# Performance work log

Hardware: AMD Instinct MI355X
Metric: run time of the kernel (lower is better)

Reference implementation:

```python
import jax, jax.numpy as jnp
import numpy as np

B, I_LEN, Q_LEN, H = 256, 256, 64, 512
MID, G, FLAT_OUT = 512, 1, 1024


def setup_inputs() -> dict:
    key = jax.random.key(0)
    ks = jax.random.split(key, 20)
    s = lambda k, sh: jax.random.normal(k, sh, dtype=jnp.float32) * 0.02
    inp = {
        'i_batch': jax.random.normal(ks[0], (B, I_LEN, H), dtype=jnp.float32),
        'q_batch': jax.random.normal(ks[1], (B, Q_LEN, H), dtype=jnp.float32),
        'i_mask': jax.random.bernoulli(ks[2], 0.1, (B, 1, 1, I_LEN)),
        'q_mask': jax.random.bernoulli(ks[3], 0.1, (B, 1, 1, Q_LEN)),
        # l_flatten (applied to i_feat) params
        'lf_w1': s(ks[4], (H, MID)), 'lf_b1': jnp.zeros((MID,), jnp.float32),
        'lf_w2': s(ks[5], (MID, G)), 'lf_b2': jnp.zeros((G,), jnp.float32),
        'lf_wm': s(ks[6], (H * G, FLAT_OUT)), 'lf_bm': jnp.zeros((FLAT_OUT,), jnp.float32),
        # i_flatten (applied to l_feat) params
        'if_w1': s(ks[7], (H, MID)), 'if_b1': jnp.zeros((MID,), jnp.float32),
        'if_w2': s(ks[8], (MID, G)), 'if_b2': jnp.zeros((G,), jnp.float32),
        'if_wm': s(ks[9], (H * G, FLAT_OUT)), 'if_bm': jnp.zeros((FLAT_OUT,), jnp.float32),
        # fh_h: Linear(1024, 512)
        'fh_w': s(ks[10], (FLAT_OUT, 512)), 'fh_b': jnp.zeros((512,), jnp.float32),
    }
    return inp


def _qkv_attention(query, key, value, mask):
    # query [B,Lq,H], key/value [B,Lk,H], mask [B,1,1,Lk] (True = pad)
    d_k = query.shape[-1]
    scores = jnp.einsum('bqh,bkh->bqk', query, key) / jnp.sqrt(jnp.asarray(d_k, query.dtype))
    scores = jnp.where(mask[:, 0], jnp.asarray(-65504.0, scores.dtype), scores)
    p_attn = jax.nn.softmax(scores, axis=-1)
    return jnp.einsum('bqk,bkh->bqh', p_attn, value)


def _att_flat(x, x_mask, w1, b1, w2, b2, wm, bm):
    # x [B,L,H], x_mask [B,1,1,L]
    att = jnp.maximum(x @ w1 + b1, 0.0) @ w2 + b2           # [B,L,G]
    att = jnp.where(x_mask[:, 0, 0, :, None], -1e9, att)
    att = jax.nn.softmax(att, axis=1)
    pooled = jnp.einsum('blg,blh->bgh', att, x).reshape(x.shape[0], -1)  # [B,G*H]
    return pooled @ wm + bm, att[..., 0]                    # att.squeeze() with G=1


def reference(i_batch, q_batch, i_mask, q_mask,
              lf_w1, lf_b1, lf_w2, lf_b2, lf_wm, lf_bm,
              if_w1, if_b1, if_w2, if_b2, if_wm, if_bm,
              fh_w, fh_b):
    i_feat = _qkv_attention(i_batch, q_batch, q_batch, q_mask)   # [B,I_LEN,H]
    i_feat, i_weight = _att_flat(i_feat, i_mask, lf_w1, lf_b1, lf_w2, lf_b2, lf_wm, lf_bm)
    l_feat = _qkv_attention(q_batch, i_batch, i_batch, i_mask)   # [B,Q_LEN,H]
    l_feat, _ = _att_flat(l_feat, q_mask, if_w1, if_b1, if_w2, if_b2, if_wm, if_bm)
    out = (l_feat + i_feat) @ fh_w + fh_b                        # [B,512]
    return out, i_weight
```

## Files before the change

### kernel.cpp

```cpp
#include <hip/hip_runtime.h>
#include <math.h>


#define SCALE 0.04419417382415922f

typedef __attribute__((ext_vector_type(8))) short short8;
typedef __attribute__((ext_vector_type(4))) float floatx4;

__device__ __forceinline__ unsigned short f2bf(float x) {
  unsigned u = __float_as_uint(x);
  unsigned r = u + 0x7FFFu + ((u >> 16) & 1u);
  return (unsigned short)(r >> 16);
}
__device__ __forceinline__ float bf2f(unsigned short h) {
  return __uint_as_float(((unsigned)h) << 16);
}
__device__ __forceinline__ unsigned pk2(float a, float b) {
  unsigned r;
  asm("v_cvt_pk_bf16_f32 %0, %1, %2" : "=v"(r) : "v"(a), "v"(b));
  return r;
}

__device__ __forceinline__ float wave_max(float v) {
#pragma unroll
  for (int o = 32; o > 0; o >>= 1) v = fmaxf(v, __shfl_xor(v, o, 64));
  return v;
}
__device__ __forceinline__ float wave_sum(float v) {
#pragma unroll
  for (int o = 32; o > 0; o >>= 1) v += __shfl_xor(v, o, 64);
  return v;
}

#define GLD_LDS16(gptr, lptr)                                             \
  __builtin_amdgcn_global_load_lds(                                       \
      (const __attribute__((address_space(1))) void*)(gptr),              \
      (__attribute__((address_space(3))) void*)(lptr), 16, 0, 0)

__global__ __launch_bounds__(256) void k_prep(
    const float* __restrict__ qb, const float* __restrict__ lf_w1,
    const float* __restrict__ if_w1, const float* __restrict__ lf_wm,
    const float* __restrict__ if_wm, const float* __restrict__ fh_w,
    unsigned short* __restrict__ qb_bf, unsigned short* __restrict__ w1t_lf,
    unsigned short* __restrict__ w1t_if, unsigned short* __restrict__ wcat_t,
    unsigned short* __restrict__ fh_wt) {
  __shared__ __align__(16) char smem[64 * 65 * 4];
  const int idx = blockIdx.x, t = threadIdx.x;

  if (idx < 512) {
    float(*T)[65] = (float(*)[65])smem;
    const float* src;
    unsigned short* dst;
    int N, ds, koff, k0, n0;
    if (idx < 64) {
      src = lf_w1; dst = w1t_lf; N = 512; ds = 512; koff = 0;
      k0 = (idx & 7) * 64; n0 = (idx >> 3) * 64;
    } else if (idx < 128) {
      int l = idx - 64;
      src = if_w1; dst = w1t_if; N = 512; ds = 512; koff = 0;
      k0 = (l & 7) * 64; n0 = (l >> 3) * 64;
    } else if (idx < 256) {
      int l = idx - 128;
      src = lf_wm; dst = wcat_t; N = 1024; ds = 1024; koff = 0;
      k0 = (l & 7) * 64; n0 = (l >> 3) * 64;
    } else if (idx < 384) {
      int l = idx - 256;
      src = if_wm; dst = wcat_t; N = 1024; ds = 1024; koff = 512;
      k0 = (l & 7) * 64; n0 = (l >> 3) * 64;
    } else {
      int l = idx - 384;
      src = fh_w; dst = fh_wt; N = 512; ds = 1024; koff = 0;
      k0 = (l & 15) * 64; n0 = (l >> 4) * 64;
    }
#pragma unroll
    for (int i = 0; i < 16; i++) {
      int e = t + i * 256, r = e >> 6, c = e & 63;
      T[r][c] = src[(size_t)(k0 + r) * N + n0 + c];
    }
    __syncthreads();
#pragma unroll
    for (int i = 0; i < 8; i++) {
      int e = t + i * 256, r = e >> 5, c2 = (e & 31) * 2;
      *(unsigned*)&dst[(size_t)(n0 + r) * ds + koff + k0 + c2] =
          pk2(T[c2][r], T[c2 + 1][r]);
    }
  } else {
    int j = idx - 512;
    const float4* src = (const float4*)(qb + (size_t)j * 4096);
    uint2* dst = (uint2*)(qb_bf + (size_t)j * 4096);
#pragma unroll
    for (int i = 0; i < 4; i++) {
      int e = t + i * 256;
      float4 v = src[e];
      uint2 p;
      p.x = pk2(v.x, v.y);
      p.y = pk2(v.z, v.w);
      dst[e] = p;
    }
  }
}

__global__ __launch_bounds__(256) void k_scores_f(
    const float* __restrict__ ib, const unsigned short* __restrict__ qbf,
    const int* __restrict__ imask, const int* __restrict__ qmask,
    unsigned short* __restrict__ P1, unsigned short* __restrict__ P2,
    float* __restrict__ psum) {
  __shared__ __align__(16) unsigned short U[64 * 64 + 128 * 64];
  unsigned short* As = U;
  unsigned short* Bs = U + 64 * 64;
  unsigned short* X = U;
  const int b = blockIdx.y, ic = blockIdx.x, i0 = ic * 128;
  const int t = threadIdx.x, w = t >> 6, lane = t & 63, c = lane & 15, qq = lane >> 4;

  floatx4 acc[4][2];
#pragma unroll
  for (int ti = 0; ti < 4; ti++)
#pragma unroll
    for (int tj = 0; tj < 2; tj++) acc[ti][tj] = (floatx4){0.f, 0.f, 0.f, 0.f};

  for (int k0 = 0; k0 < 512; k0 += 64) {
#pragma unroll
    for (int i = 0; i < 2; i++) {
      int s = i * 256 + t, row = s >> 3, src = (s & 7) ^ (row & 7);
      GLD_LDS16(qbf + ((size_t)b * 64 + row) * 512 + k0 + src * 8,
                &As[(i * 256 + w * 64) * 8]);
    }
#pragma unroll
    for (int i = 0; i < 8; i++) {
      int s = i * 256 + t, row = s >> 4, c4 = s & 15;
      float4 v = *(const float4*)&ib[((size_t)b * 256 + i0 + row) * 512 + k0 + c4 * 4];
      int gs = (c4 >> 1) ^ (row & 7), sub = c4 & 1;
      uint2 p;
      p.x = pk2(v.x, v.y);
      p.y = pk2(v.z, v.w);
      *(uint2*)&Bs[row * 64 + gs * 8 + sub * 4] = p;
    }
    __syncthreads();
#pragma unroll
    for (int kk = 0; kk < 2; kk++) {
      short8 a[4], bb[2];
#pragma unroll
      for (int ti = 0; ti < 4; ti++)
        a[ti] = *(const short8*)&As[(ti * 16 + c) * 64 + ((kk * 4 + qq) ^ (c & 7)) * 8];
#pragma unroll
      for (int tj = 0; tj < 2; tj++)
        bb[tj] = *(const short8*)&Bs[(w * 32 + tj * 16 + c) * 64 + ((kk * 4 + qq) ^ (c & 7)) * 8];
#pragma unroll
      for (int ti = 0; ti < 4; ti++)
#pragma unroll
        for (int tj = 0; tj < 2; tj++)
          acc[ti][tj] = __builtin_amdgcn_mfma_f32_16x16x32_bf16(a[ti], bb[tj], acc[ti][tj], 0, 0, 0);
    }
    __syncthreads();
  }

  const int il0 = w * 32 + c;
  int imsk0 = imask[b * 256 + i0 + il0];
  int imsk1 = imask[b * 256 + i0 + il0 + 16];
  int qm[4][4];
#pragma unroll
  for (int ti = 0; ti < 4; ti++)
#pragma unroll
    for (int rr = 0; rr < 4; rr++) qm[ti][rr] = qmask[b * 64 + ti * 16 + qq * 4 + rr];

#pragma unroll
  for (int ti = 0; ti < 4; ti++)
#pragma unroll
    for (int rr = 0; rr < 4; rr++) {
      int qv = ti * 16 + qq * 4 + rr;
      float e0 = imsk0 ? 0.f : __expf(acc[ti][0][rr] * SCALE);
      float e1 = imsk1 ? 0.f : __expf(acc[ti][1][rr] * SCALE);
      X[qv * 136 + il0] = f2bf(e0);
      X[qv * 136 + il0 + 16] = f2bf(e1);
      float s = e0 + e1;
#pragma unroll
      for (int o = 1; o <= 8; o <<= 1) s += __shfl_xor(s, o, 64);
      if (c == 0) psum[((size_t)(b * 64 + qv)) * 8 + ic * 4 + w] = s;
    }
  __syncthreads();
#pragma unroll
  for (int i = 0; i < 4; i++) {
    int e2 = t + i * 256, qv = e2 >> 4, g = e2 & 15;
    *(uint4*)&P2[((size_t)b * 64 + qv) * 256 + i0 + g * 8] = *(const uint4*)&X[qv * 136 + g * 8];
  }
  __syncthreads();

#pragma unroll
  for (int tj = 0; tj < 2; tj++) {
    float ev[4][4];
    float s1 = 0.f;
#pragma unroll
    for (int ti = 0; ti < 4; ti++)
#pragma unroll
      for (int rr = 0; rr < 4; rr++) {
        ev[ti][rr] = qm[ti][rr] ? 0.f : __expf(acc[ti][tj][rr] * SCALE);
        s1 += ev[ti][rr];
      }
    s1 += __shfl_xor(s1, 16, 64);
    s1 += __shfl_xor(s1, 32, 64);
    float inv = 1.f / s1;
    int il = il0 + tj * 16;
#pragma unroll
    for (int ti = 0; ti < 4; ti++)
#pragma unroll
      for (int rr = 0; rr < 4; rr++)
        X[il * 72 + ti * 16 + qq * 4 + rr] = f2bf(ev[ti][rr] * inv);
  }
  __syncthreads();
#pragma unroll
  for (int i = 0; i < 4; i++) {
    int e2 = t + i * 256, il = e2 >> 3, g = e2 & 7;
    *(uint4*)&P1[((size_t)b * 256 + i0 + il) * 64 + g * 8] = *(const uint4*)&X[il * 72 + g * 8];
  }
}

__global__ __launch_bounds__(256) void k_av2(const unsigned short* __restrict__ P2,
                                             const float* __restrict__ ib,
                                             const float* __restrict__ psum,
                                             unsigned short* __restrict__ lfeat) {
  __shared__ unsigned short As[64 * 64];
  __shared__ __align__(16) unsigned short Tb[128 * 64];
  const int b = blockIdx.y, n0 = blockIdx.x * 128;
  const int t = threadIdx.x, w = t >> 6, lane = t & 63, c = lane & 15, q = lane >> 4;
  const int wm = w >> 1, wn = w & 1;
  floatx4 acc[2][4];
#pragma unroll
  for (int ti = 0; ti < 2; ti++)
#pragma unroll
    for (int tj = 0; tj < 4; tj++) acc[ti][tj] = (floatx4){0.f, 0.f, 0.f, 0.f};

  for (int kc = 0; kc < 256; kc += 64) {
#pragma unroll
    for (int i = 0; i < 2; i++) {
      int s = i * 256 + t, row = s >> 3, src = (s & 7) ^ (row & 7);
      GLD_LDS16(P2 + ((size_t)b * 64 + row) * 256 + kc + src * 8, &As[(i * 256 + w * 64) * 8]);
    }
#pragma unroll
    for (int i = 0; i < 8; i++) {
      int e = i * 256 + t, tok = e >> 5, h4 = (e & 31) * 4;
      float4 v = *(const float4*)&ib[((size_t)b * 256 + kc + tok) * 512 + n0 + h4];
      uint2 p;
      p.x = pk2(v.x, v.y);
      p.y = pk2(v.z, v.w);
      int col = ((((h4 >> 3) ^ (tok >> 3)) & 15) << 3) | (h4 & 7);
      *(uint2*)&Tb[tok * 128 + col] = p;
    }
    __syncthreads();
    uint4 vv[4];
#pragma unroll
    for (int i = 0; i < 4; i++) {
      int e = i * 256 + t, h = e >> 3, tc = (e & 7) * 8;
      int hg = h >> 3, ho = h & 7;
      unsigned y[8];
#pragma unroll
      for (int k = 0; k < 8; k++) {
        int r = tc + k;
        y[k] = Tb[r * 128 + (((hg ^ (r >> 3)) & 15) << 3) + ho];
      }
      vv[i].x = y[0] | (y[1] << 16);
      vv[i].y = y[2] | (y[3] << 16);
      vv[i].z = y[4] | (y[5] << 16);
      vv[i].w = y[6] | (y[7] << 16);
    }
    __syncthreads();
#pragma unroll
    for (int i = 0; i < 4; i++) {
      int e = i * 256 + t, h = e >> 3, tc = (e & 7) * 8;
      *(uint4*)&Tb[h * 64 + (((tc >> 3) ^ (h & 7)) << 3)] = vv[i];
    }
    __syncthreads();
    const unsigned short* Bs = Tb;
#pragma unroll
    for (int kk = 0; kk < 2; kk++) {
      short8 a[2], bb[4];
#pragma unroll
      for (int ti = 0; ti < 2; ti++)
        a[ti] = *(const short8*)&As[(wm * 32 + ti * 16 + c) * 64 + ((kk * 4 + q) ^ (c & 7)) * 8];
#pragma unroll
      for (int tj = 0; tj < 4; tj++)
        bb[tj] = *(const short8*)&Bs[(wn * 64 + tj * 16 + c) * 64 + ((kk * 4 + q) ^ (c & 7)) * 8];
#pragma unroll
      for (int ti = 0; ti < 2; ti++)
#pragma unroll
        for (int tj = 0; tj < 4; tj++)
          acc[ti][tj] = __builtin_amdgcn_mfma_f32_16x16x32_bf16(a[ti], bb[tj], acc[ti][tj], 0, 0, 0);
    }
    __syncthreads();
  }
#pragma unroll
  for (int ti = 0; ti < 2; ti++)
#pragma unroll
    for (int rr = 0; rr < 4; rr++) {
      int m = wm * 32 + ti * 16 + q * 4 + rr;
      const float* ps = psum + ((size_t)(b * 64 + m)) * 8;
      float s = ps[0] + ps[1] + ps[2] + ps[3] + ps[4] + ps[5] + ps[6] + ps[7];
      float inv = 1.f / s;
      unsigned short* op = lfeat + ((size_t)b * 64 + m) * 512 + n0 + wn * 64;
#pragma unroll
      for (int tj = 0; tj < 4; tj++) op[tj * 16 + c] = f2bf(acc[ti][tj][rr] * inv);
    }
}

__global__ __launch_bounds__(256) void k_qbw1(const unsigned short* __restrict__ qbf,
                                              const unsigned short* __restrict__ W1t,
                                              unsigned short* __restrict__ qbW1T) {
  __shared__ unsigned short As[64 * 64];
  __shared__ unsigned short Bs[128 * 64];
  const int b = blockIdx.y, n0 = blockIdx.x * 128;
  const int t = threadIdx.x, w = t >> 6, lane = t & 63, c = lane & 15, q = lane >> 4;
  const int wm = w >> 1, wn = w & 1;
  floatx4 acc[2][4];
#pragma unroll
  for (int ti = 0; ti < 2; ti++)
#pragma unroll
    for (int tj = 0; tj < 4; tj++) acc[ti][tj] = (floatx4){0.f, 0.f, 0.f, 0.f};

  for (int k0 = 0; k0 < 512; k0 += 64) {
#pragma unroll
    for (int i = 0; i < 2; i++) {
      int s = i * 256 + t, row = s >> 3, src = (s & 7) ^ (row & 7);
      GLD_LDS16(qbf + ((size_t)b * 64 + row) * 512 + k0 + src * 8,
                &As[(i * 256 + w * 64) * 8]);
    }
#pragma unroll
    for (int i = 0; i < 4; i++) {
      int s = i * 256 + t, row = s >> 3, src = (s & 7) ^ (row & 7);
      GLD_LDS16(W1t + (size_t)(n0 + row) * 512 + k0 + src * 8,
                &Bs[(i * 256 + w * 64) * 8]);
    }
    __syncthreads();
#pragma unroll
    for (int kk = 0; kk < 2; kk++) {
      short8 a[2], bb[4];
#pragma unroll
      for (int ti = 0; ti < 2; ti++)
        a[ti] = *(const short8*)&As[(wm * 32 + ti * 16 + c) * 64 + ((kk * 4 + q) ^ (c & 7)) * 8];
#pragma unroll
      for (int tj = 0; tj < 4; tj++)
        bb[tj] = *(const short8*)&Bs[(wn * 64 + tj * 16 + c) * 64 + ((kk * 4 + q) ^ (c & 7)) * 8];
#pragma unroll
      for (int ti = 0; ti < 2; ti++)
#pragma unroll
        for (int tj = 0; tj < 4; tj++)
          acc[ti][tj] = __builtin_amdgcn_mfma_f32_16x16x32_bf16(a[ti], bb[tj], acc[ti][tj], 0, 0, 0);
    }
    __syncthreads();
  }
#pragma unroll
  for (int ti = 0; ti < 2; ti++)
#pragma unroll
    for (int tj = 0; tj < 4; tj++) {
      int n = n0 + wn * 64 + tj * 16 + c;
      int m = wm * 32 + ti * 16 + q * 4;
      uint2 p;
      p.x = pk2(acc[ti][tj][0], acc[ti][tj][1]);
      p.y = pk2(acc[ti][tj][2], acc[ti][tj][3]);
      *(uint2*)&qbW1T[((size_t)b * 512 + n) * 64 + m] = p;
    }
}

__global__ __launch_bounds__(256) void k_logits_i64(
    const unsigned short* __restrict__ P1, const unsigned short* __restrict__ qbW1T,
    const float* __restrict__ b1, const float* __restrict__ w2,
    float* __restrict__ outp) {
  __shared__ unsigned short As[128 * 64];
  __shared__ unsigned short Bs[128 * 64];
  __shared__ float red[2][128];
  const int b = blockIdx.y;
  const int mt = blockIdx.x & 1, nc = blockIdx.x >> 1;
  const int m0 = mt * 128, n0 = nc * 128;
  const int t = threadIdx.x, w = t >> 6, lane = t & 63, c = lane & 15, q = lane >> 4;
  const int wm = w >> 1, wn = w & 1;

#pragma unroll
  for (int i = 0; i < 4; i++) {
    int s = i * 256 + t, row = s >> 3, src = (s & 7) ^ (row & 7);
    GLD_LDS16(P1 + ((size_t)b * 256 + m0 + row) * 64 + src * 8, &As[(i * 256 + w * 64) * 8]);
  }
#pragma unroll
  for (int i = 0; i < 4; i++) {
    int s = i * 256 + t, row = s >> 3, src = (s & 7) ^ (row & 7);
    GLD_LDS16(qbW1T + ((size_t)b * 512 + n0 + row) * 64 + src * 8, &Bs[(i * 256 + w * 64) * 8]);
  }
  __syncthreads();
  floatx4 acc[4][4];
#pragma unroll
  for (int ti = 0; ti < 4; ti++)
#pragma unroll
    for (int tj = 0; tj < 4; tj++) acc[ti][tj] = (floatx4){0.f, 0.f, 0.f, 0.f};
#pragma unroll
  for (int kk = 0; kk < 2; kk++) {
    short8 a[4], bb[4];
#pragma unroll
    for (int ti = 0; ti < 4; ti++)
      a[ti] = *(const short8*)&As[(wm * 64 + ti * 16 + c) * 64 + ((kk * 4 + q) ^ (c & 7)) * 8];
#pragma unroll
    for (int tj = 0; tj < 4; tj++)
      bb[tj] = *(const short8*)&Bs[(wn * 64 + tj * 16 + c) * 64 + ((kk * 4 + q) ^ (c & 7)) * 8];
#pragma unroll
    for (int ti = 0; ti < 4; ti++)
#pragma unroll
      for (int tj = 0; tj < 4; tj++)
        acc[ti][tj] = __builtin_amdgcn_mfma_f32_16x16x32_bf16(a[ti], bb[tj], acc[ti][tj], 0, 0, 0);
  }

  float partial[4][4] = {};
#pragma unroll
  for (int tj = 0; tj < 4; tj++) {
    int n = n0 + wn * 64 + tj * 16 + c;
    float bia = b1[n], wwv = w2[n];
#pragma unroll
    for (int ti = 0; ti < 4; ti++)
#pragma unroll
      for (int r = 0; r < 4; r++)
        partial[ti][r] += fmaxf(acc[ti][tj][r] + bia, 0.f) * wwv;
  }
#pragma unroll
  for (int msk = 1; msk <= 8; msk <<= 1)
#pragma unroll
    for (int ti = 0; ti < 4; ti++)
#pragma unroll
      for (int r = 0; r < 4; r++)
        partial[ti][r] += __shfl_xor(partial[ti][r], msk, 64);
  if (c == 0) {
#pragma unroll
    for (int ti = 0; ti < 4; ti++)
#pragma unroll
      for (int r = 0; r < 4; r++)
        red[wn][wm * 64 + ti * 16 + q * 4 + r] = partial[ti][r];
  }
  __syncthreads();
  if (t < 128) outp[(size_t)nc * 65536 + b * 256 + m0 + t] = red[0][t] + red[1][t];
}

__global__ __launch_bounds__(256) void k_logits_part(
    const unsigned short* __restrict__ X, const unsigned short* __restrict__ W1t,
    const float* __restrict__ b1, const float* __restrict__ w2,
    float* __restrict__ outp, int M) {
  __shared__ unsigned short As[128 * 64];
  __shared__ unsigned short Bs[128 * 64];
  __shared__ float red[2][128];
  const int t = threadIdx.x, w = t >> 6, lane = t & 63;
  const int wm = w >> 1, wn = w & 1, c = lane & 15, q = lane >> 4;
  const int idx = blockIdx.x;
  const int m_tile = (idx & 7) + ((idx >> 5) << 3), nc = (idx >> 3) & 3;
  const int m0 = m_tile * 128, n0 = nc * 128;

  floatx4 acc[4][4];
#pragma unroll
  for (int ti = 0; ti < 4; ti++)
#pragma unroll
    for (int tj = 0; tj < 4; tj++) acc[ti][tj] = (floatx4){0.f, 0.f, 0.f, 0.f};

  for (int k0 = 0; k0 < 512; k0 += 64) {
#pragma unroll
    for (int it = 0; it < 4; it++) {
      int s = it * 256 + t, row = s >> 3, src = (s & 7) ^ (row & 7);
      GLD_LDS16(X + (size_t)(m0 + row) * 512 + k0 + src * 8, &As[(it * 256 + w * 64) * 8]);
      GLD_LDS16(W1t + (size_t)(n0 + row) * 512 + k0 + src * 8, &Bs[(it * 256 + w * 64) * 8]);
    }
    __syncthreads();
#pragma unroll
    for (int kk = 0; kk < 2; kk++) {
      short8 a[4], bb[4];
#pragma unroll
      for (int ti = 0; ti < 4; ti++)
        a[ti] = *(const short8*)&As[(wm * 64 + ti * 16 + c) * 64 + ((kk * 4 + q) ^ (c & 7)) * 8];
#pragma unroll
      for (int tj = 0; tj < 4; tj++)
        bb[tj] = *(const short8*)&Bs[(wn * 64 + tj * 16 + c) * 64 + ((kk * 4 + q) ^ (c & 7)) * 8];
#pragma unroll
      for (int ti = 0; ti < 4; ti++)
#pragma unroll
        for (int tj = 0; tj < 4; tj++)
          acc[ti][tj] = __builtin_amdgcn_mfma_f32_16x16x32_bf16(a[ti], bb[tj], acc[ti][tj], 0, 0, 0);
    }
    __syncthreads();
  }
  float partial[4][4] = {};
#pragma unroll
  for (int tj = 0; tj < 4; tj++) {
    int n = n0 + wn * 64 + tj * 16 + c;
    float bia = b1[n], wwv = w2[n];
#pragma unroll
    for (int ti = 0; ti < 4; ti++)
#pragma unroll
      for (int r = 0; r < 4; r++)
        partial[ti][r] += fmaxf(acc[ti][tj][r] + bia, 0.f) * wwv;
  }
#pragma unroll
  for (int msk = 1; msk <= 8; msk <<= 1)
#pragma unroll
    for (int ti = 0; ti < 4; ti++)
#pragma unroll
      for (int r = 0; r < 4; r++)
        partial[ti][r] += __shfl_xor(partial[ti][r], msk, 64);
  if (c == 0) {
#pragma unroll
    for (int ti = 0; ti < 4; ti++)
#pragma unroll
      for (int r = 0; r < 4; r++)
        red[wn][wm * 64 + ti * 16 + q * 4 + r] = partial[ti][r];
  }
  __syncthreads();
  if (t < 128) outp[(size_t)nc * M + m0 + t] = red[0][t] + red[1][t];
}

__global__ __launch_bounds__(256) void k_final(const float* __restrict__ lp_i,
                                               const float* __restrict__ lp_l,
                                               const int* __restrict__ imask,
                                               const int* __restrict__ qmask,
                                               const unsigned short* __restrict__ P1,
                                               const unsigned short* __restrict__ qbf,
                                               const unsigned short* __restrict__ lfeat,
                                               float* __restrict__ iw_out,
                                               unsigned short* __restrict__ pooled) {
  __shared__ float red4[4];
  __shared__ float ar[256];
  __shared__ float red[4][64];
  __shared__ float vsm[64];
  const int t = threadIdx.x;
  if (blockIdx.x < 256) {
    const int b = blockIdx.x;
    const int i = b * 256 + t;
    float x = lp_i[i] + lp_i[65536 + i] + lp_i[131072 + i] + lp_i[196608 + i];
    float v = imask[i] ? -1e9f : x;
    float wmx = wave_max(v);
    if ((t & 63) == 0) red4[t >> 6] = wmx;
    __syncthreads();
    float mx = fmaxf(fmaxf(red4[0], red4[1]), fmaxf(red4[2], red4[3]));
    __syncthreads();
    float e = __expf(v - mx);
    float ws = wave_sum(e);
    if ((t & 63) == 0) red4[t >> 6] = ws;
    __syncthreads();
    float s = red4[0] + red4[1] + red4[2] + red4[3];
    float p = e / s;
    iw_out[i] = p;
    ar[t] = p;
    __syncthreads();
    const int part = t >> 6, lane = t & 63;
    const unsigned short* Pb = P1 + ((size_t)b * 256 + part * 64) * 64 + lane;
    float s0 = 0.f, s1 = 0.f;
#pragma unroll 8
    for (int ii = 0; ii < 64; ii += 2) {
      s0 += ar[part * 64 + ii] * bf2f(Pb[(size_t)ii * 64]);
      s1 += ar[part * 64 + ii + 1] * bf2f(Pb[(size_t)(ii + 1) * 64]);
    }
    red[part][lane] = s0 + s1;
    __syncthreads();
    if (t < 64) vsm[t] = red[0][t] + red[1][t] + red[2][t] + red[3][t];
    __syncthreads();
    float a0 = 0.f, a1 = 0.f;
    const unsigned short* Xb = qbf + (size_t)b * 64 * 512 + 2 * t;
#pragma unroll 4
    for (int l = 0; l < 64; l++) {
      unsigned u = *(const unsigned*)&Xb[(size_t)l * 512];
      float a = vsm[l];
      a0 += a * bf2f((unsigned short)(u & 0xffff));
      a1 += a * bf2f((unsigned short)(u >> 16));
    }
    *(unsigned*)&pooled[(size_t)b * 1024 + 2 * t] = pk2(a0, a1);
  } else {
    const int b = blockIdx.x - 256;
    if (t < 64) {
      const int i = b * 64 + t;
      float x = lp_l[i] + lp_l[16384 + i] + lp_l[32768 + i] + lp_l[49152 + i];
      float v = qmask[i] ? -1e9f : x;
      float mx = wave_max(v);
      float e = __expf(v - mx);
      float s = wave_sum(e);
      ar[t] = e / s;
    }
    __syncthreads();
    float a0 = 0.f, a1 = 0.f;
    const unsigned short* Xb = lfeat + (size_t)b * 64 * 512 + 2 * t;
#pragma unroll 4
    for (int l = 0; l < 64; l++) {
      unsigned u = *(const unsigned*)&Xb[(size_t)l * 512];
      float a = ar[l];
      a0 += a * bf2f((unsigned short)(u & 0xffff));
      a1 += a * bf2f((unsigned short)(u >> 16));
    }
    *(unsigned*)&pooled[(size_t)b * 1024 + 512 + 2 * t] = pk2(a0, a1);
  }
}

__global__ __launch_bounds__(256) void k_egemm(const unsigned short* __restrict__ X,
                                               const unsigned short* __restrict__ Wt,
                                               const float* __restrict__ biasA,
                                               const float* __restrict__ biasB,
                                               float* __restrict__ outf,
                                               unsigned short* __restrict__ outbf,
                                               int N, int K) {
  __shared__ unsigned short As[64 * 64];
  __shared__ unsigned short Bs[64 * 64];
  const int n0 = blockIdx.x * 64, m0 = blockIdx.y * 64;
  const int t = threadIdx.x, w = t >> 6, lane = t & 63, c = lane & 15, q = lane >> 4;
  const int wm = w >> 1, wn = w & 1;
  floatx4 acc[2][2];
#pragma unroll
  for (int ti = 0; ti < 2; ti++)
#pragma unroll
    for (int tj = 0; tj < 2; tj++) acc[ti][tj] = (floatx4){0.f, 0.f, 0.f, 0.f};

  for (int k0 = 0; k0 < K; k0 += 64) {
#pragma unroll
    for (int i = 0; i < 2; i++) {
      int s = i * 256 + t, row = s >> 3, src = (s & 7) ^ (row & 7);
      GLD_LDS16(X + (size_t)(m0 + row) * K + k0 + src * 8, &As[(i * 256 + w * 64) * 8]);
      GLD_LDS16(Wt + (size_t)(n0 + row) * K + k0 + src * 8, &Bs[(i * 256 + w * 64) * 8]);
    }
    __syncthreads();
#pragma unroll
    for (int kk = 0; kk < 2; kk++) {
      short8 a[2], bb[2];
#pragma unroll
      for (int ti = 0; ti < 2; ti++)
        a[ti] = *(const short8*)&As[(wm * 32 + ti * 16 + c) * 64 + ((kk * 4 + q) ^ (c & 7)) * 8];
#pragma unroll
      for (int tj = 0; tj < 2; tj++)
        bb[tj] = *(const short8*)&Bs[(wn * 32 + tj * 16 + c) * 64 + ((kk * 4 + q) ^ (c & 7)) * 8];
#pragma unroll
      for (int ti = 0; ti < 2; ti++)
#pragma unroll
        for (int tj = 0; tj < 2; tj++)
          acc[ti][tj] = __builtin_amdgcn_mfma_f32_16x16x32_bf16(a[ti], bb[tj], acc[ti][tj], 0, 0, 0);
    }
    __syncthreads();
  }
#pragma unroll
  for (int tj = 0; tj < 2; tj++) {
    int n = n0 + wn * 32 + tj * 16 + c;
    float bias = biasA[n] + (biasB ? biasB[n] : 0.f);
#pragma unroll
    for (int ti = 0; ti < 2; ti++)
#pragma unroll
      for (int rr = 0; rr < 4; rr++) {
        int m = m0 + wm * 32 + ti * 16 + q * 4 + rr;
        float v = acc[ti][tj][rr] + bias;
        if (outbf) outbf[(size_t)m * N + n] = f2bf(v);
        else outf[(size_t)m * N + n] = v;
      }
  }
}

extern "C" void kernel_launch(void* const* d_in, const int* in_sizes, int n_in,
                              void* d_out, int out_size, void* d_ws, size_t ws_size,
                              hipStream_t stream) {
  const float* ib = (const float*)d_in[0];
  const float* qb = (const float*)d_in[1];
  const int* imask = (const int*)d_in[2];
  const int* qmask = (const int*)d_in[3];
  const float* lf_w1 = (const float*)d_in[4];
  const float* lf_b1 = (const float*)d_in[5];
  const float* lf_w2 = (const float*)d_in[6];
  const float* lf_wm = (const float*)d_in[8];
  const float* lf_bm = (const float*)d_in[9];
  const float* if_w1 = (const float*)d_in[10];
  const float* if_b1 = (const float*)d_in[11];
  const float* if_w2 = (const float*)d_in[12];
  const float* if_wm = (const float*)d_in[14];
  const float* if_bm = (const float*)d_in[15];
  const float* fh_w = (const float*)d_in[16];
  const float* fh_b = (const float*)d_in[17];
  float* out = (float*)d_out;

  float* lp_i = (float*)d_ws;
  float* lp_l = lp_i + 262144;
  float* att_i = lp_l + 65536;
  float* att_l = att_i + 65536;
  float* psum = att_l + 16384;
  unsigned short* P1 = (unsigned short*)(psum + 131072);
  unsigned short* P2 = P1 + 4194304;
  unsigned short* lfeat = P2 + 4194304;
  unsigned short* qb_bf = lfeat + 33554432;
  unsigned short* qbW1T = qb_bf + 8388608;
  unsigned short* ibT_unused = qbW1T + 8388608;
  unsigned short* w1t_lf = ibT_unused + 33554432;
  unsigned short* w1t_if = w1t_lf + 262144;
  unsigned short* wcat_t = w1t_if + 262144;
  unsigned short* fh_wt = wcat_t + 1048576;
  unsigned short* pooled_bf = fh_wt + 524288;
  unsigned short* F_bf = pooled_bf + 262144;

  k_prep<<<2560, 256, 0, stream>>>(qb, lf_w1, if_w1, lf_wm, if_wm, fh_w,
                                   qb_bf, w1t_lf, w1t_if, wcat_t, fh_wt);

  k_scores_f<<<dim3(2, 256), 256, 0, stream>>>(ib, qb_bf, imask, qmask, P1, P2, psum);
  k_av2<<<dim3(4, 256), 256, 0, stream>>>(P2, ib, psum, lfeat);
  k_qbw1<<<dim3(4, 256), 256, 0, stream>>>(qb_bf, w1t_lf, qbW1T);
  k_logits_i64<<<dim3(8, 256), 256, 0, stream>>>(P1, qbW1T, lf_b1, lf_w2, lp_i);
  k_logits_part<<<512, 256, 0, stream>>>(lfeat, w1t_if, if_b1, if_w2, lp_l, 16384);
  k_final<<<512, 256, 0, stream>>>(lp_i, lp_l, imask, qmask, P1, qb_bf, lfeat,
                                   out + 131072, pooled_bf);

  k_egemm<<<dim3(16, 4), 256, 0, stream>>>(pooled_bf, wcat_t, lf_bm, if_bm,
                                           nullptr, F_bf, 1024, 1024);
  k_egemm<<<dim3(8, 4), 256, 0, stream>>>(F_bf, fh_wt, fh_b, nullptr,
                                          out, nullptr, 512, 1024);
}
```

Before: 371.5 us.

## Fuse qb·W1 GEMM into logits kernel and register-prefetch tiles in scores/av

```diff
diff --git a/kernel.cpp b/kernel.cpp
--- a/kernel.cpp
+++ b/kernel.cpp
@@ -118,22 +118,46 @@
 #pragma unroll
     for (int tj = 0; tj < 2; tj++) acc[ti][tj] = (floatx4){0.f, 0.f, 0.f, 0.f};
 
+  uint4 qa[2];
+  float4 vb[8];
+#pragma unroll
+  for (int i = 0; i < 2; i++) {
+    int s = i * 256 + t, row = s >> 3, srcg = (s & 7) ^ (row & 7);
+    qa[i] = *(const uint4*)&qbf[((size_t)b * 64 + row) * 512 + srcg * 8];
+  }
+#pragma unroll
+  for (int i = 0; i < 8; i++) {
+    int s = i * 256 + t, row = s >> 4, c4 = s & 15;
+    vb[i] = *(const float4*)&ib[((size_t)b * 256 + i0 + row) * 512 + c4 * 4];
+  }
+
   for (int k0 = 0; k0 < 512; k0 += 64) {
 #pragma unroll
     for (int i = 0; i < 2; i++) {
-      int s = i * 256 + t, row = s >> 3, src = (s & 7) ^ (row & 7);
-      GLD_LDS16(qbf + ((size_t)b * 64 + row) * 512 + k0 + src * 8,
-                &As[(i * 256 + w * 64) * 8]);
+      int s = i * 256 + t;
+      *(uint4*)&As[s * 8] = qa[i];
     }
 #pragma unroll
     for (int i = 0; i < 8; i++) {
       int s = i * 256 + t, row = s >> 4, c4 = s & 15;
-      float4 v = *(const float4*)&ib[((size_t)b * 256 + i0 + row) * 512 + k0 + c4 * 4];
       int gs = (c4 >> 1) ^ (row & 7), sub = c4 & 1;
       uint2 p;
-      p.x = pk2(v.x, v.y);
-      p.y = pk2(v.z, v.w);
+      p.x = pk2(vb[i].x, vb[i].y);
+      p.y = pk2(vb[i].z, vb[i].w);
       *(uint2*)&Bs[row * 64 + gs * 8 + sub * 4] = p;
+    }
+    if (k0 < 448) {
+      int kn = k0 + 64;
+#pragma unroll
+      for (int i = 0; i < 2; i++) {
+        int s = i * 256 + t, row = s >> 3, srcg = (s & 7) ^ (row & 7);
+        qa[i] = *(const uint4*)&qbf[((size_t)b * 64 + row) * 512 + kn + srcg * 8];
+      }
+#pragma unroll
+      for (int i = 0; i < 8; i++) {
+        int s = i * 256 + t, row = s >> 4, c4 = s & 15;
+        vb[i] = *(const float4*)&ib[((size_t)b * 256 + i0 + row) * 512 + kn + c4 * 4];
+      }
     }
     __syncthreads();
 #pragma unroll
@@ -229,21 +253,46 @@
 #pragma unroll
     for (int tj = 0; tj < 4; tj++) acc[ti][tj] = (floatx4){0.f, 0.f, 0.f, 0.f};
 
+  uint4 pa[2];
+  float4 vb[8];
+#pragma unroll
+  for (int i = 0; i < 2; i++) {
+    int s = i * 256 + t, row = s >> 3, srcg = (s & 7) ^ (row & 7);
+    pa[i] = *(const uint4*)&P2[((size_t)b * 64 + row) * 256 + srcg * 8];
+  }
+#pragma unroll
+  for (int i = 0; i < 8; i++) {
+    int e = i * 256 + t, tok = e >> 5, h4 = (e & 31) * 4;
+    vb[i] = *(const float4*)&ib[((size_t)b * 256 + tok) * 512 + n0 + h4];
+  }
+
   for (int kc = 0; kc < 256; kc += 64) {
 #pragma unroll
     for (int i = 0; i < 2; i++) {
-      int s = i * 256 + t, row = s >> 3, src = (s & 7) ^ (row & 7);
-      GLD_LDS16(P2 + ((size_t)b * 64 + row) * 256 + kc + src * 8, &As[(i * 256 + w * 64) * 8]);
+      int s = i * 256 + t;
+      *(uint4*)&As[s * 8] = pa[i];
     }
 #pragma unroll
     for (int i = 0; i < 8; i++) {
       int e = i * 256 + t, tok = e >> 5, h4 = (e & 31) * 4;
-      float4 v = *(const float4*)&ib[((size_t)b * 256 + kc + tok) * 512 + n0 + h4];
       uint2 p;
-      p.x = pk2(v.x, v.y);
-      p.y = pk2(v.z, v.w);
+      p.x = pk2(vb[i].x, vb[i].y);
+      p.y = pk2(vb[i].z, vb[i].w);
       int col = ((((h4 >> 3) ^ (tok >> 3)) & 15) << 3) | (h4 & 7);
       *(uint2*)&Tb[tok * 128 + col] = p;
+    }
+    if (kc < 192) {
+      int kn = kc + 64;
+#pragma unroll
+      for (int i = 0; i < 2; i++) {
+        int s = i * 256 + t, row = s >> 3, srcg = (s & 7) ^ (row & 7);
+        pa[i] = *(const uint4*)&P2[((size_t)b * 64 + row) * 256 + kn + srcg * 8];
+      }
+#pragma unroll
+      for (int i = 0; i < 8; i++) {
+        int e = i * 256 + t, tok = e >> 5, h4 = (e & 31) * 4;
+        vb[i] = *(const float4*)&ib[((size_t)b * 256 + kn + tok) * 512 + n0 + h4];
+      }
     }
     __syncthreads();
     uint4 vv[4];
@@ -301,14 +350,20 @@
     }
 }
 
-__global__ __launch_bounds__(256) void k_qbw1(const unsigned short* __restrict__ qbf,
-                                              const unsigned short* __restrict__ W1t,
-                                              unsigned short* __restrict__ qbW1T) {
-  __shared__ unsigned short As[64 * 64];
-  __shared__ unsigned short Bs[128 * 64];
-  const int b = blockIdx.y, n0 = blockIdx.x * 128;
+__global__ __launch_bounds__(256) void k_logits_i(
+    const unsigned short* __restrict__ qbf, const unsigned short* __restrict__ W1t,
+    const unsigned short* __restrict__ P1, const float* __restrict__ b1,
+    const float* __restrict__ w2, float* __restrict__ outp) {
+  __shared__ __align__(16) unsigned short U[16384];
+  __shared__ float red[2][128];
+  unsigned short* As = U;
+  unsigned short* Bs = U + 4096;
+  unsigned short* Bs2 = U;
+  unsigned short* As2 = U + 8192;
+  const int b = blockIdx.y, nc = blockIdx.x, n0 = nc * 128;
   const int t = threadIdx.x, w = t >> 6, lane = t & 63, c = lane & 15, q = lane >> 4;
   const int wm = w >> 1, wn = w & 1;
+
   floatx4 acc[2][4];
 #pragma unroll
   for (int ti = 0; ti < 2; ti++)
@@ -346,91 +401,78 @@
     }
     __syncthreads();
   }
+
 #pragma unroll
   for (int ti = 0; ti < 2; ti++)
 #pragma unroll
     for (int tj = 0; tj < 4; tj++) {
-      int n = n0 + wn * 64 + tj * 16 + c;
-      int m = wm * 32 + ti * 16 + q * 4;
+      int nl = wn * 64 + tj * 16 + c;
+      int qb_ = wm * 32 + ti * 16 + q * 4;
       uint2 p;
       p.x = pk2(acc[ti][tj][0], acc[ti][tj][1]);
       p.y = pk2(acc[ti][tj][2], acc[ti][tj][3]);
-      *(uint2*)&qbW1T[((size_t)b * 512 + n) * 64 + m] = p;
-    }
-}
-
-__global__ __launch_bounds__(256) void k_logits_i64(
-    const unsigned short* __restrict__ P1, const unsigned short* __restrict__ qbW1T,
-    const float* __restrict__ b1, const float* __restrict__ w2,
-    float* __restrict__ outp) {
-  __shared__ unsigned short As[128 * 64];
-  __shared__ unsigned short Bs[128 * 64];
-  __shared__ float red[2][128];
-  const int b = blockIdx.y;
-  const int mt = blockIdx.x & 1, nc = blockIdx.x >> 1;
-  const int m0 = mt * 128, n0 = nc * 128;
-  const int t = threadIdx.x, w = t >> 6, lane = t & 63, c = lane & 15, q = lane >> 4;
-  const int wm = w >> 1, wn = w & 1;
-
-#pragma unroll
-  for (int i = 0; i < 4; i++) {
-    int s = i * 256 + t, row = s >> 3, src = (s & 7) ^ (row & 7);
-    GLD_LDS16(P1 + ((size_t)b * 256 + m0 + row) * 64 + src * 8, &As[(i * 256 + w * 64) * 8]);
-  }
-#pragma unroll
-  for (int i = 0; i < 4; i++) {
-    int s = i * 256 + t, row = s >> 3, src = (s & 7) ^ (row & 7);
-    GLD_LDS16(qbW1T + ((size_t)b * 512 + n0 + row) * 64 + src * 8, &Bs[(i * 256 + w * 64) * 8]);
-  }
-  __syncthreads();
-  floatx4 acc[4][4];
-#pragma unroll
-  for (int ti = 0; ti < 4; ti++)
-#pragma unroll
-    for (int tj = 0; tj < 4; tj++) acc[ti][tj] = (floatx4){0.f, 0.f, 0.f, 0.f};
-#pragma unroll
-  for (int kk = 0; kk < 2; kk++) {
-    short8 a[4], bb[4];
+      *(uint2*)&Bs2[nl * 64 + (((qb_ >> 3) ^ (nl & 7)) << 3) + (qb_ & 7)] = p;
+    }
+
+  for (int mt = 0; mt < 2; mt++) {
+    const int m0 = mt * 128;
+#pragma unroll
+    for (int i = 0; i < 4; i++) {
+      int s = i * 256 + t, row = s >> 3, src = (s & 7) ^ (row & 7);
+      GLD_LDS16(P1 + ((size_t)b * 256 + m0 + row) * 64 + src * 8,
+                &As2[(i * 256 + w * 64) * 8]);
+    }
+    __syncthreads();
+    floatx4 acc2[4][4];
 #pragma unroll
     for (int ti = 0; ti < 4; ti++)
-      a[ti] = *(const short8*)&As[(wm * 64 + ti * 16 + c) * 64 + ((kk * 4 + q) ^ (c & 7)) * 8];
-#pragma unroll
-    for (int tj = 0; tj < 4; tj++)
-      bb[tj] = *(const short8*)&Bs[(wn * 64 + tj * 16 + c) * 64 + ((kk * 4 + q) ^ (c & 7)) * 8];
-#pragma unroll
-    for (int ti = 0; ti < 4; ti++)
+#pragma unroll
+      for (int tj = 0; tj < 4; tj++) acc2[ti][tj] = (floatx4){0.f, 0.f, 0.f, 0.f};
+#pragma unroll
+    for (int kk = 0; kk < 2; kk++) {
+      short8 a[4], bb[4];
+#pragma unroll
+      for (int ti = 0; ti < 4; ti++)
+        a[ti] = *(const short8*)&As2[(wm * 64 + ti * 16 + c) * 64 + ((kk * 4 + q) ^ (c & 7)) * 8];
 #pragma unroll
       for (int tj = 0; tj < 4; tj++)
-        acc[ti][tj] = __builtin_amdgcn_mfma_f32_16x16x32_bf16(a[ti], bb[tj], acc[ti][tj], 0, 0, 0);
-  }
-
-  float partial[4][4] = {};
-#pragma unroll
-  for (int tj = 0; tj < 4; tj++) {
-    int n = n0 + wn * 64 + tj * 16 + c;
-    float bia = b1[n], wwv = w2[n];
-#pragma unroll
-    for (int ti = 0; ti < 4; ti++)
-#pragma unroll
-      for (int r = 0; r < 4; r++)
-        partial[ti][r] += fmaxf(acc[ti][tj][r] + bia, 0.f) * wwv;
-  }
-#pragma unroll
-  for (int msk = 1; msk <= 8; msk <<= 1)
-#pragma unroll
-    for (int ti = 0; ti < 4; ti++)
-#pragma unroll
-      for (int r = 0; r < 4; r++)
-        partial[ti][r] += __shfl_xor(partial[ti][r], msk, 64);
-  if (c == 0) {
-#pragma unroll
-    for (int ti = 0; ti < 4; ti++)
-#pragma unroll
-      for (int r = 0; r < 4; r++)
-        red[wn][wm * 64 + ti * 16 + q * 4 + r] = partial[ti][r];
-  }
-  __syncthreads();
-  if (t < 128) outp[(size_t)nc * 65536 + b * 256 + m0 + t] = red[0][t] + red[1][t];
+        bb[tj] = *(const short8*)&Bs2[(wn * 64 + tj * 16 + c) * 64 + ((kk * 4 + q) ^ (c & 7)) * 8];
+#pragma unroll
+      for (int ti = 0; ti < 4; ti++)
+#pragma unroll
+        for (int tj = 0; tj < 4; tj++)
+          acc2[ti][tj] = __builtin_amdgcn_mfma_f32_16x16x32_bf16(a[ti], bb[tj], acc2[ti][tj], 0, 0, 0);
+    }
+
+    float partial[4][4] = {};
+#pragma unroll
+    for (int tj = 0; tj < 4; tj++) {
+      int n = n0 + wn * 64 + tj * 16 + c;
+      float bia = b1[n], wwv = w2[n];
+#pragma unroll
+      for (int ti = 0; ti < 4; ti++)
+#pragma unroll
+        for (int r = 0; r < 4; r++)
+          partial[ti][r] += fmaxf(acc2[ti][tj][r] + bia, 0.f) * wwv;
+    }
+#pragma unroll
+    for (int msk = 1; msk <= 8; msk <<= 1)
+#pragma unroll
+      for (int ti = 0; ti < 4; ti++)
+#pragma unroll
+        for (int r = 0; r < 4; r++)
+          partial[ti][r] += __shfl_xor(partial[ti][r], msk, 64);
+    if (c == 0) {
+#pragma unroll
+      for (int ti = 0; ti < 4; ti++)
+#pragma unroll
+        for (int r = 0; r < 4; r++)
+          red[wn][wm * 64 + ti * 16 + q * 4 + r] = partial[ti][r];
+    }
+    __syncthreads();
+    if (t < 128) outp[(size_t)nc * 65536 + b * 256 + m0 + t] = red[0][t] + red[1][t];
+    __syncthreads();
+  }
 }
 
 __global__ __launch_bounds__(256) void k_logits_part(
@@ -675,8 +717,8 @@
   unsigned short* P2 = P1 + 4194304;
   unsigned short* lfeat = P2 + 4194304;
   unsigned short* qb_bf = lfeat + 33554432;
-  unsigned short* qbW1T = qb_bf + 8388608;
-  unsigned short* ibT_unused = qbW1T + 8388608;
+  unsigned short* qbW1T_unused = qb_bf + 8388608;
+  unsigned short* ibT_unused = qbW1T_unused + 8388608;
   unsigned short* w1t_lf = ibT_unused + 33554432;
   unsigned short* w1t_if = w1t_lf + 262144;
   unsigned short* wcat_t = w1t_if + 262144;
@@ -689,8 +731,7 @@
 
   k_scores_f<<<dim3(2, 256), 256, 0, stream>>>(ib, qb_bf, imask, qmask, P1, P2, psum);
   k_av2<<<dim3(4, 256), 256, 0, stream>>>(P2, ib, psum, lfeat);
-  k_qbw1<<<dim3(4, 256), 256, 0, stream>>>(qb_bf, w1t_lf, qbW1T);
-  k_logits_i64<<<dim3(8, 256), 256, 0, stream>>>(P1, qbW1T, lf_b1, lf_w2, lp_i);
+  k_logits_i<<<dim3(4, 256), 256, 0, stream>>>(qb_bf, w1t_lf, P1, lf_b1, lf_w2, lp_i);
   k_logits_part<<<512, 256, 0, stream>>>(lfeat, w1t_if, if_b1, if_w2, lp_l, 16384);
   k_final<<<512, 256, 0, stream>>>(lp_i, lp_l, imask, qmask, P1, qb_bf, lfeat,
                                    out + 131072, pooled_bf);
```

Result: no change. 371.3 us (-0.0%).
